# Optimization experiments

Hardware: AMD Instinct MI355X
Metric: run time of the kernel (lower is better)

Reference implementation:

```python
import jax, jax.numpy as jnp
import numpy as np

NUM_STEPS = 3  # matches init_kwargs num_steps
UNITS = 256
N_STRUCT = 4096
N_ATOMS_TOTAL = 131072
FEAT_IN = 256


def setup_inputs() -> dict:
    key = jax.random.key(0)
    ks = jax.random.split(key, 7)
    field = jax.random.normal(ks[0], (N_ATOMS_TOTAL, FEAT_IN), dtype=jnp.float32)
    # Dense(units) params
    Wd = jax.random.normal(ks[1], (FEAT_IN, UNITS), dtype=jnp.float32) / np.sqrt(FEAT_IN)
    bd = jnp.zeros((UNITS,), dtype=jnp.float32)
    # Keras LSTM params: kernel [2*units, 4*units], recurrent [units, 4*units], bias [4*units]
    Wk = jax.random.normal(ks[2], (2 * UNITS, 4 * UNITS), dtype=jnp.float32) / np.sqrt(2 * UNITS)
    Wr = jax.random.normal(ks[3], (UNITS, 4 * UNITS), dtype=jnp.float32) / np.sqrt(UNITS)
    b_lstm = jnp.zeros((4 * UNITS,), dtype=jnp.float32)
    # sorted segment ids = get_segment_indices_from_n(counts)
    segment_ids = jnp.sort(jax.random.randint(ks[4], (N_ATOMS_TOTAL,), 0, N_STRUCT)).astype(jnp.int32)
    return {"field": field, "Wd": Wd, "bd": bd, "Wk": Wk, "Wr": Wr,
            "b_lstm": b_lstm, "segment_ids": segment_ids, "n_struct": N_STRUCT}


def _segment_softmax(e, seg, num_segments):
    # per-channel softmax within each segment (matches unsorted_segment_softmax)
    m = jax.ops.segment_max(e, seg, num_segments=num_segments)
    ex = jnp.exp(e - m[seg])
    s = jax.ops.segment_sum(ex, seg, num_segments=num_segments)
    return ex / s[seg]


def _lstm_step(x, h, c, Wk, Wr, b):
    # Keras gate order: i, f, g(c), o
    z = x @ Wk + h @ Wr + b
    i, f, g, o = jnp.split(z, 4, axis=-1)
    c_new = jax.nn.sigmoid(f) * c + jax.nn.sigmoid(i) * jnp.tanh(g)
    h_new = jax.nn.sigmoid(o) * jnp.tanh(c_new)
    return h_new, c_new


def reference(field, Wd, bd, Wk, Wr, b_lstm, segment_ids, n_struct):
    units = Wd.shape[1]
    x = field @ Wd + bd                              # [N_atoms, units]
    q_star = jnp.zeros((n_struct, 2 * units), dtype=x.dtype)
    h = jnp.zeros((n_struct, units), dtype=x.dtype)
    c = jnp.zeros((n_struct, units), dtype=x.dtype)
    for _ in range(NUM_STEPS):
        h, c = _lstm_step(q_star, h, c, Wk, Wr, b_lstm)
        qt = h                                        # [n_struct, units]
        eit = x * qt[segment_ids]                     # gather == tf.repeat(qt, counts)
        ait = _segment_softmax(eit, segment_ids, n_struct)
        rt = jax.ops.segment_sum(ait * x, segment_ids, num_segments=n_struct)
        q_star = jnp.concatenate([qt, rt], axis=-1)   # [n_struct, 2*units]
    return q_star
```

## Files before the change

### kernel.cpp

```cpp
#include <hip/hip_runtime.h>
#include <math.h>

#define N_ATOMS   131072
#define FEAT      256
#define UNITS     256
#define NSTRUCT   4096
#define ZDIM      1024
#define QDIM      512
#define KLSTM     768
#define LDP       40

typedef __attribute__((ext_vector_type(8))) __bf16 bf16x8;
typedef __attribute__((ext_vector_type(4))) float  f32x4;

__device__ __forceinline__ float sigm(float v) { return 1.0f / (1.0f + __expf(-v)); }

__device__ __forceinline__ unsigned short bf16_rne(float v) {
    unsigned int u = __float_as_uint(v);
    u += 0x7fffu + ((u >> 16) & 1u);
    return (unsigned short)(u >> 16);
}
__device__ __forceinline__ float bf16_f32(unsigned short b) {
    return __uint_as_float(((unsigned int)b) << 16);
}
__device__ __forceinline__ bf16x8 frag_ld(const unsigned short* p) {
    uint4 u = *(const uint4*)p;
    bf16x8 r; __builtin_memcpy(&r, &u, 16); return r;
}

__global__ void seg_offs_kernel(const int* __restrict__ seg, int* __restrict__ offs) {
    int s = blockIdx.x * blockDim.x + threadIdx.x;
    if (s > NSTRUCT) return;
    int lo = 0, hi = N_ATOMS;
    while (lo < hi) {
        int mid = (lo + hi) >> 1;
        if (seg[mid] < s) lo = mid + 1; else hi = mid;
    }
    offs[s] = lo;
}

__global__ __launch_bounds__(256) void prep_wd_kernel(
    const float* __restrict__ Wd, unsigned short* __restrict__ Th,
    unsigned short* __restrict__ Tl)
{
    int t = blockIdx.x * 256 + threadIdx.x;
    int k = t >> 8, n = t & 255;
    float v = Wd[t];
    unsigned short h = bf16_rne(v);
    unsigned short l = bf16_rne(v - bf16_f32(h));
    Th[n * FEAT + k] = h;
    Tl[n * FEAT + k] = l;
}

__global__ __launch_bounds__(256) void prep_wlstm_kernel(
    const float* __restrict__ Wk, const float* __restrict__ Wr,
    unsigned short* __restrict__ Th, unsigned short* __restrict__ Tl)
{
    int t = blockIdx.x * 256 + threadIdx.x;
    int k = t >> 10, n = t & 1023;
    float v = (k < QDIM) ? Wk[t] : Wr[t - QDIM * ZDIM];
    unsigned short h = bf16_rne(v);
    unsigned short l = bf16_rne(v - bf16_f32(h));
    Th[n * KLSTM + k] = h;
    Tl[n * KLSTM + k] = l;
}

__global__ __launch_bounds__(256) void gemm_x_mfma(
    const float* __restrict__ A,
    const unsigned short* __restrict__ BTh,
    const unsigned short* __restrict__ BTl,
    const float* __restrict__ bias, float* __restrict__ C)
{
    __shared__ unsigned short Ah[128][LDP], Al[128][LDP];
    __shared__ unsigned short Bh[128][LDP], Bl[128][LDP];
    const int bn = blockIdx.x * 128;
    const int bm = blockIdx.y * 128;
    const int t  = threadIdx.x;
    const int w  = t >> 6, l = t & 63;
    const int wr = w & 1, wc = w >> 1;
    const int lm = l & 15, koff = (l >> 4) * 8;

    f32x4 acc[4][4] = {};

    for (int k0 = 0; k0 < FEAT; k0 += 32) {
        #pragma unroll
        for (int i = 0; i < 2; ++i) {
            int flat = t + i * 256;
            int n = flat >> 2, kc = flat & 3;
            *(uint4*)&Bh[n][kc * 8] = *(const uint4*)&BTh[(size_t)(bn + n) * FEAT + k0 + kc * 8];
            *(uint4*)&Bl[n][kc * 8] = *(const uint4*)&BTl[(size_t)(bn + n) * FEAT + k0 + kc * 8];
        }
        #pragma unroll
        for (int i = 0; i < 4; ++i) {
            int flat = t + i * 256;
            int m = flat >> 3, kq = flat & 7;
            const float4 v = *(const float4*)&A[(size_t)(bm + m) * FEAT + k0 + kq * 4];
            unsigned short h0 = bf16_rne(v.x), h1 = bf16_rne(v.y);
            unsigned short h2 = bf16_rne(v.z), h3 = bf16_rne(v.w);
            unsigned short l0 = bf16_rne(v.x - bf16_f32(h0));
            unsigned short l1 = bf16_rne(v.y - bf16_f32(h1));
            unsigned short l2 = bf16_rne(v.z - bf16_f32(h2));
            unsigned short l3 = bf16_rne(v.w - bf16_f32(h3));
            uint2 hw, lw;
            hw.x = (unsigned)h0 | ((unsigned)h1 << 16);
            hw.y = (unsigned)h2 | ((unsigned)h3 << 16);
            lw.x = (unsigned)l0 | ((unsigned)l1 << 16);
            lw.y = (unsigned)l2 | ((unsigned)l3 << 16);
            *(uint2*)&Ah[m][kq * 4] = hw;
            *(uint2*)&Al[m][kq * 4] = lw;
        }
        __syncthreads();
        bf16x8 ah[4], al[4];
        #pragma unroll
        for (int i = 0; i < 4; ++i) {
            ah[i] = frag_ld(&Ah[wr * 64 + i * 16 + lm][koff]);
            al[i] = frag_ld(&Al[wr * 64 + i * 16 + lm][koff]);
        }
        #pragma unroll
        for (int j = 0; j < 4; ++j) {
            bf16x8 bh = frag_ld(&Bh[wc * 64 + j * 16 + lm][koff]);
            bf16x8 bl = frag_ld(&Bl[wc * 64 + j * 16 + lm][koff]);
            #pragma unroll
            for (int i = 0; i < 4; ++i) {
                acc[i][j] = __builtin_amdgcn_mfma_f32_16x16x32_bf16(ah[i], bh, acc[i][j], 0, 0, 0);
                acc[i][j] = __builtin_amdgcn_mfma_f32_16x16x32_bf16(al[i], bh, acc[i][j], 0, 0, 0);
                acc[i][j] = __builtin_amdgcn_mfma_f32_16x16x32_bf16(ah[i], bl, acc[i][j], 0, 0, 0);
            }
        }
        __syncthreads();
    }

    const int lg4 = (l >> 4) * 4;
    #pragma unroll
    for (int i = 0; i < 4; ++i)
        #pragma unroll
        for (int j = 0; j < 4; ++j) {
            int col  = bn + wc * 64 + j * 16 + lm;
            int row0 = bm + wr * 64 + i * 16 + lg4;
            float bb = bias[col];
            #pragma unroll
            for (int r = 0; r < 4; ++r)
                C[(size_t)(row0 + r) * FEAT + col] = acc[i][j][r] + bb;
        }
}

__global__ __launch_bounds__(256) void lstm_gemm_mfma(
    const float* __restrict__ qstar, const float* __restrict__ hsrc,
    const unsigned short* __restrict__ BTh,
    const unsigned short* __restrict__ BTl,
    const float* __restrict__ bias, float* __restrict__ z)
{
    __shared__ unsigned short Ah[128][LDP], Al[128][LDP];
    __shared__ unsigned short Bh[128][LDP], Bl[128][LDP];
    const int bn = blockIdx.x * 128;
    const int bm = blockIdx.y * 128;
    const int t  = threadIdx.x;
    const int w  = t >> 6, l = t & 63;
    const int wr = w & 1, wc = w >> 1;
    const int lm = l & 15, koff = (l >> 4) * 8;

    f32x4 acc[4][4] = {};

    for (int k0 = 0; k0 < KLSTM; k0 += 32) {
        #pragma unroll
        for (int i = 0; i < 2; ++i) {
            int flat = t + i * 256;
            int n = flat >> 2, kc = flat & 3;
            *(uint4*)&Bh[n][kc * 8] = *(const uint4*)&BTh[(size_t)(bn + n) * KLSTM + k0 + kc * 8];
            *(uint4*)&Bl[n][kc * 8] = *(const uint4*)&BTl[(size_t)(bn + n) * KLSTM + k0 + kc * 8];
        }
        const float* Asrc; int lda, kb;
        if (k0 < QDIM) { Asrc = qstar; lda = QDIM;  kb = k0; }
        else           { Asrc = hsrc;  lda = UNITS; kb = k0 - QDIM; }
        #pragma unroll
        for (int i = 0; i < 4; ++i) {
            int flat = t + i * 256;
            int m = flat >> 3, kq = flat & 7;
            const float4 v = *(const float4*)&Asrc[(size_t)(bm + m) * lda + kb + kq * 4];
            unsigned short h0 = bf16_rne(v.x), h1 = bf16_rne(v.y);
            unsigned short h2 = bf16_rne(v.z), h3 = bf16_rne(v.w);
            unsigned short l0 = bf16_rne(v.x - bf16_f32(h0));
            unsigned short l1 = bf16_rne(v.y - bf16_f32(h1));
            unsigned short l2 = bf16_rne(v.z - bf16_f32(h2));
            unsigned short l3 = bf16_rne(v.w - bf16_f32(h3));
            uint2 hw, lw;
            hw.x = (unsigned)h0 | ((unsigned)h1 << 16);
            hw.y = (unsigned)h2 | ((unsigned)h3 << 16);
            lw.x = (unsigned)l0 | ((unsigned)l1 << 16);
            lw.y = (unsigned)l2 | ((unsigned)l3 << 16);
            *(uint2*)&Ah[m][kq * 4] = hw;
            *(uint2*)&Al[m][kq * 4] = lw;
        }
        __syncthreads();
        bf16x8 ah[4], al[4];
        #pragma unroll
        for (int i = 0; i < 4; ++i) {
            ah[i] = frag_ld(&Ah[wr * 64 + i * 16 + lm][koff]);
            al[i] = frag_ld(&Al[wr * 64 + i * 16 + lm][koff]);
        }
        #pragma unroll
        for (int j = 0; j < 4; ++j) {
            bf16x8 bh = frag_ld(&Bh[wc * 64 + j * 16 + lm][koff]);
            bf16x8 bl = frag_ld(&Bl[wc * 64 + j * 16 + lm][koff]);
            #pragma unroll
            for (int i = 0; i < 4; ++i) {
                acc[i][j] = __builtin_amdgcn_mfma_f32_16x16x32_bf16(ah[i], bh, acc[i][j], 0, 0, 0);
                acc[i][j] = __builtin_amdgcn_mfma_f32_16x16x32_bf16(al[i], bh, acc[i][j], 0, 0, 0);
                acc[i][j] = __builtin_amdgcn_mfma_f32_16x16x32_bf16(ah[i], bl, acc[i][j], 0, 0, 0);
            }
        }
        __syncthreads();
    }

    const int lg4 = (l >> 4) * 4;
    #pragma unroll
    for (int i = 0; i < 4; ++i)
        #pragma unroll
        for (int j = 0; j < 4; ++j) {
            int col  = bn + wc * 64 + j * 16 + lm;
            int row0 = bm + wr * 64 + i * 16 + lg4;
            float bb = bias[col];
            #pragma unroll
            for (int r = 0; r < 4; ++r)
                z[(size_t)(row0 + r) * ZDIM + col] = acc[i][j][r] + bb;
        }
}

__global__ __launch_bounds__(256) void gates_kernel(
    const float* __restrict__ z, const float* __restrict__ c_in,
    float* __restrict__ h_out, float* __restrict__ c_out)
{
    int idx = blockIdx.x * 256 + threadIdx.x;
    int s = idx >> 8, ch = idx & 255;
    const float* zr = z + (size_t)s * ZDIM;
    float zi = zr[ch], zf = zr[256 + ch], zg = zr[512 + ch], zo = zr[768 + ch];
    float cold = c_in[idx];
    float cn = sigm(zf) * cold + sigm(zi) * tanhf(zg);
    float hn = sigm(zo) * tanhf(cn);
    h_out[idx] = hn;
    c_out[idx] = cn;
}

__global__ void h1c1_kernel(const float* __restrict__ b, float* __restrict__ hc_rows) {
    int ch = threadIdx.x;
    float zi = b[ch], zg = b[512 + ch], zo = b[768 + ch];
    float cn = sigm(zi) * tanhf(zg);
    float hn = sigm(zo) * tanhf(cn);
    hc_rows[ch] = hn;
    hc_rows[256 + ch] = cn;
}

__global__ __launch_bounds__(256) void bcast_kernel(
    const float* __restrict__ hc_rows, float* __restrict__ h, float* __restrict__ c)
{
    int idx = blockIdx.x * 256 + threadIdx.x;
    int ch = idx & 255;
    h[idx] = hc_rows[ch];
    c[idx] = hc_rows[256 + ch];
}

__global__ __launch_bounds__(1024) void attn_kernel(
    const float* __restrict__ x, const float* __restrict__ h,
    const int* __restrict__ offs, float* __restrict__ qstar_out)
{
    __shared__ float Lm[4][UNITS], Ls[4][UNITS], Lr[4][UNITS];
    const int s  = blockIdx.x;
    const int t  = threadIdx.x;
    const int ch = t & 255;
    const int p  = t >> 8;
    const float q = h[(size_t)s * UNITS + ch];
    const int a0 = offs[s], a1 = offs[s + 1];

    float m = -INFINITY, ssum = 0.0f, r = 0.0f;
    int a = a0 + p;
    for (; a + 12 < a1; a += 16) {
        float x0 = x[(size_t)(a +  0) * FEAT + ch];
        float x1 = x[(size_t)(a +  4) * FEAT + ch];
        float x2 = x[(size_t)(a +  8) * FEAT + ch];
        float x3 = x[(size_t)(a + 12) * FEAT + ch];
        float e0 = x0 * q, e1 = x1 * q, e2 = x2 * q, e3 = x3 * q;
        float mn = fmaxf(fmaxf(fmaxf(e0, e1), fmaxf(e2, e3)), m);
        float sc = __expf(m - mn);
        float p0 = __expf(e0 - mn), p1 = __expf(e1 - mn);
        float p2 = __expf(e2 - mn), p3 = __expf(e3 - mn);
        ssum = ssum * sc + ((p0 + p1) + (p2 + p3));
        r    = r    * sc + ((p0 * x0 + p1 * x1) + (p2 * x2 + p3 * x3));
        m = mn;
    }
    for (; a < a1; a += 4) {
        float xv = x[(size_t)a * FEAT + ch];
        float e = xv * q;
        float mn = fmaxf(m, e);
        float sc = __expf(m - mn);
        float pe = __expf(e - mn);
        ssum = ssum * sc + pe;
        r = r * sc + pe * xv;
        m = mn;
    }
    Lm[p][ch] = m; Ls[p][ch] = ssum; Lr[p][ch] = r;
    __syncthreads();

    if (p == 0) {
        float m0 = Lm[0][ch], m1 = Lm[1][ch], m2 = Lm[2][ch], m3 = Lm[3][ch];
        float ms = fmaxf(fmaxf(m0, m1), fmaxf(m2, m3));
        float rt = 0.0f;
        if (a1 > a0) {
            float w0 = __expf(m0 - ms), w1 = __expf(m1 - ms);
            float w2 = __expf(m2 - ms), w3 = __expf(m3 - ms);
            float S = Ls[0][ch] * w0 + Ls[1][ch] * w1 + Ls[2][ch] * w2 + Ls[3][ch] * w3;
            float R = Lr[0][ch] * w0 + Lr[1][ch] * w1 + Lr[2][ch] * w2 + Lr[3][ch] * w3;
            rt = R / S;
        }
        qstar_out[(size_t)s * QDIM + ch] = q;
        qstar_out[(size_t)s * QDIM + UNITS + ch] = rt;
    }
}

extern "C" void kernel_launch(void* const* d_in, const int* in_sizes, int n_in,
                              void* d_out, int out_size, void* d_ws, size_t ws_size,
                              hipStream_t stream) {
    const float* field  = (const float*)d_in[0];
    const float* Wd     = (const float*)d_in[1];
    const float* bd     = (const float*)d_in[2];
    const float* Wk     = (const float*)d_in[3];
    const float* Wr     = (const float*)d_in[4];
    const float* b_lstm = (const float*)d_in[5];
    const int*   segids = (const int*)d_in[6];

    float* ws   = (float*)d_ws;
    float* x    = ws;
    float* z    = x + (size_t)N_ATOMS * FEAT;
    float* qst  = z + (size_t)NSTRUCT * ZDIM;
    float* h    = qst + (size_t)NSTRUCT * QDIM;
    float* c    = h + (size_t)NSTRUCT * UNITS;
    float* hcr  = c + (size_t)NSTRUCT * UNITS;
    int*   offs = (int*)(hcr + 512);

    unsigned short* wdt_h = (unsigned short*)d_out;
    unsigned short* wdt_l = wdt_h + 256 * 256;
    unsigned short* wt_h  = wdt_l + 256 * 256;
    unsigned short* wt_l  = wt_h + 1024 * 768;

    seg_offs_kernel<<<(NSTRUCT + 1 + 255) / 256, 256, 0, stream>>>(segids, offs);
    prep_wd_kernel<<<256, 256, 0, stream>>>(Wd, wdt_h, wdt_l);
    prep_wlstm_kernel<<<3072, 256, 0, stream>>>(Wk, Wr, wt_h, wt_l);

    gemm_x_mfma<<<dim3(FEAT / 128, N_ATOMS / 128), 256, 0, stream>>>(
        field, wdt_h, wdt_l, bd, x);

    h1c1_kernel<<<1, 256, 0, stream>>>(b_lstm, hcr);
    bcast_kernel<<<NSTRUCT, 256, 0, stream>>>(hcr, h, c);
    attn_kernel<<<NSTRUCT, 1024, 0, stream>>>(x, h, offs, qst);

    for (int step = 1; step < 3; ++step) {
        lstm_gemm_mfma<<<dim3(ZDIM / 128, NSTRUCT / 128), 256, 0, stream>>>(
            qst, h, wt_h, wt_l, b_lstm, z);
        gates_kernel<<<NSTRUCT, 256, 0, stream>>>(z, c, h, c);
        float* qdst = (step == 2) ? (float*)d_out : qst;
        attn_kernel<<<NSTRUCT, 1024, 0, stream>>>(x, h, offs, qdst);
    }
}
```

Measured before the change: 447.5 us.

## Fold recurrent weights into LSTM kernel, fuse gates into attention, prefetch GEMM tiles

The LSTM input h always equals the first half of q_star, so Wr is added into the first 256 rows of Wk. This shrinks the LSTM GEMM K from 768 to 512 and drops the separate h buffer. The gates computation and the initial h/c broadcast are fused into the attention kernel, which removes the gates, h1c1 and bcast launches and their global round trips. One GEMM kernel with register prefetch of A and direct global-to-LDS loads of B replaces both GEMMs, which risks LDS bank conflicts because the B tile padding is removed.

```diff
diff --git a/kernel.cpp b/kernel.cpp
--- a/kernel.cpp
+++ b/kernel.cpp
@@ -7,7 +7,7 @@
 #define NSTRUCT   4096
 #define ZDIM      1024
 #define QDIM      512
-#define KLSTM     768
+#define KLSTM     512
 #define LDP       40
 
 typedef __attribute__((ext_vector_type(8))) __bf16 bf16x8;
@@ -26,6 +26,11 @@
 __device__ __forceinline__ bf16x8 frag_ld(const unsigned short* p) {
     uint4 u = *(const uint4*)p;
     bf16x8 r; __builtin_memcpy(&r, &u, 16); return r;
+}
+__device__ __forceinline__ void gload16(const unsigned short* g, unsigned short* l) {
+    __builtin_amdgcn_global_load_lds(
+        (const __attribute__((address_space(1))) unsigned int*)g,
+        (__attribute__((address_space(3))) unsigned int*)l, 16, 0, 0);
 }
 
 __global__ void seg_offs_kernel(const int* __restrict__ seg, int* __restrict__ offs) {
@@ -58,21 +63,22 @@
 {
     int t = blockIdx.x * 256 + threadIdx.x;
     int k = t >> 10, n = t & 1023;
-    float v = (k < QDIM) ? Wk[t] : Wr[t - QDIM * ZDIM];
+    float v = Wk[(size_t)k * ZDIM + n];
+    if (k < 256) v += Wr[(size_t)k * ZDIM + n];
     unsigned short h = bf16_rne(v);
     unsigned short l = bf16_rne(v - bf16_f32(h));
-    Th[n * KLSTM + k] = h;
-    Tl[n * KLSTM + k] = l;
-}
-
-__global__ __launch_bounds__(256) void gemm_x_mfma(
-    const float* __restrict__ A,
+    Th[(size_t)n * KLSTM + k] = h;
+    Tl[(size_t)n * KLSTM + k] = l;
+}
+
+__global__ __launch_bounds__(256) void gemm_split(
+    const float* __restrict__ A, int lda, int K,
     const unsigned short* __restrict__ BTh,
     const unsigned short* __restrict__ BTl,
-    const float* __restrict__ bias, float* __restrict__ C)
+    const float* __restrict__ bias, float* __restrict__ C, int ldc)
 {
     __shared__ unsigned short Ah[128][LDP], Al[128][LDP];
-    __shared__ unsigned short Bh[128][LDP], Bl[128][LDP];
+    __shared__ unsigned short Bh[128 * 32], Bl[128 * 32];
     const int bn = blockIdx.x * 128;
     const int bm = blockIdx.y * 128;
     const int t  = threadIdx.x;
@@ -81,20 +87,28 @@
     const int lm = l & 15, koff = (l >> 4) * 8;
 
     f32x4 acc[4][4] = {};
-
-    for (int k0 = 0; k0 < FEAT; k0 += 32) {
-        #pragma unroll
-        for (int i = 0; i < 2; ++i) {
-            int flat = t + i * 256;
-            int n = flat >> 2, kc = flat & 3;
-            *(uint4*)&Bh[n][kc * 8] = *(const uint4*)&BTh[(size_t)(bn + n) * FEAT + k0 + kc * 8];
-            *(uint4*)&Bl[n][kc * 8] = *(const uint4*)&BTl[(size_t)(bn + n) * FEAT + k0 + kc * 8];
-        }
+    float4 pa[4];
+
+    #pragma unroll
+    for (int i = 0; i < 2; ++i) {
+        int flat = t + i * 256;
+        int n = flat >> 2, kc = flat & 3;
+        gload16(&BTh[(size_t)(bn + n) * K + kc * 8], &Bh[(size_t)(w * 64 + i * 256) * 8]);
+        gload16(&BTl[(size_t)(bn + n) * K + kc * 8], &Bl[(size_t)(w * 64 + i * 256) * 8]);
+    }
+    #pragma unroll
+    for (int i = 0; i < 4; ++i) {
+        int flat = t + i * 256;
+        int m = flat >> 3, kq = flat & 7;
+        pa[i] = *(const float4*)&A[(size_t)(bm + m) * lda + kq * 4];
+    }
+
+    for (int k0 = 0; k0 < K; k0 += 32) {
         #pragma unroll
         for (int i = 0; i < 4; ++i) {
             int flat = t + i * 256;
             int m = flat >> 3, kq = flat & 7;
-            const float4 v = *(const float4*)&A[(size_t)(bm + m) * FEAT + k0 + kq * 4];
+            float4 v = pa[i];
             unsigned short h0 = bf16_rne(v.x), h1 = bf16_rne(v.y);
             unsigned short h2 = bf16_rne(v.z), h3 = bf16_rne(v.w);
             unsigned short l0 = bf16_rne(v.x - bf16_f32(h0));
@@ -110,6 +124,17 @@
             *(uint2*)&Al[m][kq * 4] = lw;
         }
         __syncthreads();
+
+        const bool more = (k0 + 32) < K;
+        if (more) {
+            #pragma unroll
+            for (int i = 0; i < 4; ++i) {
+                int flat = t + i * 256;
+                int m = flat >> 3, kq = flat & 7;
+                pa[i] = *(const float4*)&A[(size_t)(bm + m) * lda + k0 + 32 + kq * 4];
+            }
+        }
+
         bf16x8 ah[4], al[4];
         #pragma unroll
         for (int i = 0; i < 4; ++i) {
@@ -118,8 +143,8 @@
         }
         #pragma unroll
         for (int j = 0; j < 4; ++j) {
-            bf16x8 bh = frag_ld(&Bh[wc * 64 + j * 16 + lm][koff]);
-            bf16x8 bl = frag_ld(&Bl[wc * 64 + j * 16 + lm][koff]);
+            bf16x8 bh = frag_ld(&Bh[(size_t)(wc * 64 + j * 16 + lm) * 32 + koff]);
+            bf16x8 bl = frag_ld(&Bl[(size_t)(wc * 64 + j * 16 + lm) * 32 + koff]);
             #pragma unroll
             for (int i = 0; i < 4; ++i) {
                 acc[i][j] = __builtin_amdgcn_mfma_f32_16x16x32_bf16(ah[i], bh, acc[i][j], 0, 0, 0);
@@ -128,6 +153,17 @@
             }
         }
         __syncthreads();
+        if (more) {
+            #pragma unroll
+            for (int i = 0; i < 2; ++i) {
+                int flat = t + i * 256;
+                int n = flat >> 2, kc = flat & 3;
+                gload16(&BTh[(size_t)(bn + n) * K + k0 + 32 + kc * 8],
+                        &Bh[(size_t)(w * 64 + i * 256) * 8]);
+                gload16(&BTl[(size_t)(bn + n) * K + k0 + 32 + kc * 8],
+                        &Bl[(size_t)(w * 64 + i * 256) * 8]);
+            }
+        }
     }
 
     const int lg4 = (l >> 4) * 4;
@@ -140,135 +176,40 @@
             float bb = bias[col];
             #pragma unroll
             for (int r = 0; r < 4; ++r)
-                C[(size_t)(row0 + r) * FEAT + col] = acc[i][j][r] + bb;
-        }
-}
-
-__global__ __launch_bounds__(256) void lstm_gemm_mfma(
-    const float* __restrict__ qstar, const float* __restrict__ hsrc,
-    const unsigned short* __restrict__ BTh,
-    const unsigned short* __restrict__ BTl,
-    const float* __restrict__ bias, float* __restrict__ z)
-{
-    __shared__ unsigned short Ah[128][LDP], Al[128][LDP];
-    __shared__ unsigned short Bh[128][LDP], Bl[128][LDP];
-    const int bn = blockIdx.x * 128;
-    const int bm = blockIdx.y * 128;
-    const int t  = threadIdx.x;
-    const int w  = t >> 6, l = t & 63;
-    const int wr = w & 1, wc = w >> 1;
-    const int lm = l & 15, koff = (l >> 4) * 8;
-
-    f32x4 acc[4][4] = {};
-
-    for (int k0 = 0; k0 < KLSTM; k0 += 32) {
-        #pragma unroll
-        for (int i = 0; i < 2; ++i) {
-            int flat = t + i * 256;
-            int n = flat >> 2, kc = flat & 3;
-            *(uint4*)&Bh[n][kc * 8] = *(const uint4*)&BTh[(size_t)(bn + n) * KLSTM + k0 + kc * 8];
-            *(uint4*)&Bl[n][kc * 8] = *(const uint4*)&BTl[(size_t)(bn + n) * KLSTM + k0 + kc * 8];
-        }
-        const float* Asrc; int lda, kb;
-        if (k0 < QDIM) { Asrc = qstar; lda = QDIM;  kb = k0; }
-        else           { Asrc = hsrc;  lda = UNITS; kb = k0 - QDIM; }
-        #pragma unroll
-        for (int i = 0; i < 4; ++i) {
-            int flat = t + i * 256;
-            int m = flat >> 3, kq = flat & 7;
-            const float4 v = *(const float4*)&Asrc[(size_t)(bm + m) * lda + kb + kq * 4];
-            unsigned short h0 = bf16_rne(v.x), h1 = bf16_rne(v.y);
-            unsigned short h2 = bf16_rne(v.z), h3 = bf16_rne(v.w);
-            unsigned short l0 = bf16_rne(v.x - bf16_f32(h0));
-            unsigned short l1 = bf16_rne(v.y - bf16_f32(h1));
-            unsigned short l2 = bf16_rne(v.z - bf16_f32(h2));
-            unsigned short l3 = bf16_rne(v.w - bf16_f32(h3));
-            uint2 hw, lw;
-            hw.x = (unsigned)h0 | ((unsigned)h1 << 16);
-            hw.y = (unsigned)h2 | ((unsigned)h3 << 16);
-            lw.x = (unsigned)l0 | ((unsigned)l1 << 16);
-            lw.y = (unsigned)l2 | ((unsigned)l3 << 16);
-            *(uint2*)&Ah[m][kq * 4] = hw;
-            *(uint2*)&Al[m][kq * 4] = lw;
-        }
-        __syncthreads();
-        bf16x8 ah[4], al[4];
-        #pragma unroll
-        for (int i = 0; i < 4; ++i) {
-            ah[i] = frag_ld(&Ah[wr * 64 + i * 16 + lm][koff]);
-            al[i] = frag_ld(&Al[wr * 64 + i * 16 + lm][koff]);
-        }
-        #pragma unroll
-        for (int j = 0; j < 4; ++j) {
-            bf16x8 bh = frag_ld(&Bh[wc * 64 + j * 16 + lm][koff]);
-            bf16x8 bl = frag_ld(&Bl[wc * 64 + j * 16 + lm][koff]);
-            #pragma unroll
-            for (int i = 0; i < 4; ++i) {
-                acc[i][j] = __builtin_amdgcn_mfma_f32_16x16x32_bf16(ah[i], bh, acc[i][j], 0, 0, 0);
-                acc[i][j] = __builtin_amdgcn_mfma_f32_16x16x32_bf16(al[i], bh, acc[i][j], 0, 0, 0);
-                acc[i][j] = __builtin_amdgcn_mfma_f32_16x16x32_bf16(ah[i], bl, acc[i][j], 0, 0, 0);
-            }
-        }
-        __syncthreads();
-    }
-
-    const int lg4 = (l >> 4) * 4;
-    #pragma unroll
-    for (int i = 0; i < 4; ++i)
-        #pragma unroll
-        for (int j = 0; j < 4; ++j) {
-            int col  = bn + wc * 64 + j * 16 + lm;
-            int row0 = bm + wr * 64 + i * 16 + lg4;
-            float bb = bias[col];
-            #pragma unroll
-            for (int r = 0; r < 4; ++r)
-                z[(size_t)(row0 + r) * ZDIM + col] = acc[i][j][r] + bb;
-        }
-}
-
-__global__ __launch_bounds__(256) void gates_kernel(
-    const float* __restrict__ z, const float* __restrict__ c_in,
-    float* __restrict__ h_out, float* __restrict__ c_out)
-{
-    int idx = blockIdx.x * 256 + threadIdx.x;
-    int s = idx >> 8, ch = idx & 255;
-    const float* zr = z + (size_t)s * ZDIM;
-    float zi = zr[ch], zf = zr[256 + ch], zg = zr[512 + ch], zo = zr[768 + ch];
-    float cold = c_in[idx];
-    float cn = sigm(zf) * cold + sigm(zi) * tanhf(zg);
-    float hn = sigm(zo) * tanhf(cn);
-    h_out[idx] = hn;
-    c_out[idx] = cn;
-}
-
-__global__ void h1c1_kernel(const float* __restrict__ b, float* __restrict__ hc_rows) {
-    int ch = threadIdx.x;
-    float zi = b[ch], zg = b[512 + ch], zo = b[768 + ch];
-    float cn = sigm(zi) * tanhf(zg);
-    float hn = sigm(zo) * tanhf(cn);
-    hc_rows[ch] = hn;
-    hc_rows[256 + ch] = cn;
-}
-
-__global__ __launch_bounds__(256) void bcast_kernel(
-    const float* __restrict__ hc_rows, float* __restrict__ h, float* __restrict__ c)
-{
-    int idx = blockIdx.x * 256 + threadIdx.x;
-    int ch = idx & 255;
-    h[idx] = hc_rows[ch];
-    c[idx] = hc_rows[256 + ch];
-}
-
-__global__ __launch_bounds__(1024) void attn_kernel(
-    const float* __restrict__ x, const float* __restrict__ h,
-    const int* __restrict__ offs, float* __restrict__ qstar_out)
-{
+                C[(size_t)(row0 + r) * ldc + col] = acc[i][j][r] + bb;
+        }
+}
+
+__global__ __launch_bounds__(1024) void attn_fused(
+    const float* __restrict__ x, const float* __restrict__ zsrc, int use_z,
+    float* __restrict__ c, const int* __restrict__ offs,
+    float* __restrict__ qstar_out)
+{
+    __shared__ float hq[UNITS];
     __shared__ float Lm[4][UNITS], Ls[4][UNITS], Lr[4][UNITS];
     const int s  = blockIdx.x;
     const int t  = threadIdx.x;
     const int ch = t & 255;
     const int p  = t >> 8;
-    const float q = h[(size_t)s * UNITS + ch];
+
+    if (p == 0) {
+        float zi, zf, zg, zo, cold;
+        if (use_z) {
+            const float* zr = zsrc + (size_t)s * ZDIM;
+            zi = zr[ch]; zf = zr[256 + ch]; zg = zr[512 + ch]; zo = zr[768 + ch];
+            cold = c[(size_t)s * UNITS + ch];
+        } else {
+            zi = zsrc[ch]; zf = zsrc[256 + ch]; zg = zsrc[512 + ch]; zo = zsrc[768 + ch];
+            cold = 0.0f;
+        }
+        float cn = sigm(zf) * cold + sigm(zi) * tanhf(zg);
+        float hn = sigm(zo) * tanhf(cn);
+        c[(size_t)s * UNITS + ch] = cn;
+        hq[ch] = hn;
+    }
+    __syncthreads();
+
+    const float q = hq[ch];
     const int a0 = offs[s], a1 = offs[s + 1];
 
     float m = -INFINITY, ssum = 0.0f, r = 0.0f;
@@ -331,32 +272,27 @@
     float* x    = ws;
     float* z    = x + (size_t)N_ATOMS * FEAT;
     float* qst  = z + (size_t)NSTRUCT * ZDIM;
-    float* h    = qst + (size_t)NSTRUCT * QDIM;
-    float* c    = h + (size_t)NSTRUCT * UNITS;
-    float* hcr  = c + (size_t)NSTRUCT * UNITS;
-    int*   offs = (int*)(hcr + 512);
+    float* c    = qst + (size_t)NSTRUCT * QDIM;
+    int*   offs = (int*)(c + (size_t)NSTRUCT * UNITS);
 
     unsigned short* wdt_h = (unsigned short*)d_out;
     unsigned short* wdt_l = wdt_h + 256 * 256;
     unsigned short* wt_h  = wdt_l + 256 * 256;
-    unsigned short* wt_l  = wt_h + 1024 * 768;
+    unsigned short* wt_l  = wt_h + (size_t)ZDIM * KLSTM;
 
     seg_offs_kernel<<<(NSTRUCT + 1 + 255) / 256, 256, 0, stream>>>(segids, offs);
     prep_wd_kernel<<<256, 256, 0, stream>>>(Wd, wdt_h, wdt_l);
-    prep_wlstm_kernel<<<3072, 256, 0, stream>>>(Wk, Wr, wt_h, wt_l);
-
-    gemm_x_mfma<<<dim3(FEAT / 128, N_ATOMS / 128), 256, 0, stream>>>(
-        field, wdt_h, wdt_l, bd, x);
-
-    h1c1_kernel<<<1, 256, 0, stream>>>(b_lstm, hcr);
-    bcast_kernel<<<NSTRUCT, 256, 0, stream>>>(hcr, h, c);
-    attn_kernel<<<NSTRUCT, 1024, 0, stream>>>(x, h, offs, qst);
+    prep_wlstm_kernel<<<ZDIM * KLSTM / 256, 256, 0, stream>>>(Wk, Wr, wt_h, wt_l);
+
+    gemm_split<<<dim3(FEAT / 128, N_ATOMS / 128), 256, 0, stream>>>(
+        field, FEAT, FEAT, wdt_h, wdt_l, bd, x, FEAT);
+
+    attn_fused<<<NSTRUCT, 1024, 0, stream>>>(x, b_lstm, 0, c, offs, qst);
 
     for (int step = 1; step < 3; ++step) {
-        lstm_gemm_mfma<<<dim3(ZDIM / 128, NSTRUCT / 128), 256, 0, stream>>>(
-            qst, h, wt_h, wt_l, b_lstm, z);
-        gates_kernel<<<NSTRUCT, 256, 0, stream>>>(z, c, h, c);
+        gemm_split<<<dim3(ZDIM / 128, NSTRUCT / 128), 256, 0, stream>>>(
+            qst, KLSTM, KLSTM, wt_h, wt_l, b_lstm, z, ZDIM);
         float* qdst = (step == 2) ? (float*)d_out : qst;
-        attn_kernel<<<NSTRUCT, 1024, 0, stream>>>(x, h, offs, qdst);
-    }
-}
+        attn_fused<<<NSTRUCT, 1024, 0, stream>>>(x, z, 1, c, offs, qdst);
+    }
+}
```

Result: faster. 413.7 us (-7.6%).
